# Kernel tuning notes

Measured on AMD Instinct MI355X. Metric: run time of the kernel, lower is better.

The kernel has to match this reference:

```python
import jax, jax.numpy as jnp
import numpy as np


def _log_g(x):
    # log of g(x) = x + 0.5 for x >= 0, sigmoid(x) for x < 0 (minGRU paper, log-space)
    return jnp.where(x >= 0, jnp.log(jax.nn.relu(x) + 0.5), -jax.nn.softplus(-x))


def setup_inputs() -> dict:
    key = jax.random.key(0)
    k1, k2, k3 = jax.random.split(key, 3)
    B, L, D, H = 4, 8192, 512, 1024
    x = jax.random.normal(k1, (B, L, D), dtype=jnp.float32)
    # 1x1 conv in-projection to [hidden | gate], scaled for sane activation magnitudes
    W_in = jax.random.normal(k2, (2 * H, D), dtype=jnp.float32) * 0.05
    b_in = jnp.zeros((2 * H,), dtype=jnp.float32)
    # 1x1 conv out-projection back to model dim
    W_out = jax.random.normal(k3, (D, H), dtype=jnp.float32) * 0.05
    b_out = jnp.zeros((D,), dtype=jnp.float32)
    return {"x": x, "W_in": W_in, "b_in": b_in, "W_out": W_out, "b_out": b_out}


def reference(x, W_in, b_in, W_out, b_out):
    # x: [B, L, D]. tokenMixer transposes to [B, D, L] for MinGRU (1x1 convs),
    # which is equivalent to pointwise matmuls over the channel dim here.
    hg = jnp.einsum('bld,ed->ble', x, W_in) + b_in          # [B, L, 2H]
    H = hg.shape[-1] // 2
    hidden, gate = hg[..., :H], hg[..., H:]

    # minGRU log-space parallel scan (Heinsen associative scan):
    # h_t = (1 - z_t) * h_{t-1} + z_t * g(hidden_t), z_t = sigmoid(gate_t)
    log_coeffs = -jax.nn.softplus(gate)      # log(1 - z_t)
    log_z = -jax.nn.softplus(-gate)          # log(z_t)
    log_tilde_h = _log_g(hidden)             # log(g(hidden_t))

    a_star = jnp.cumsum(log_coeffs, axis=1)                              # [B, L, H]
    log_h = a_star + jax.lax.cumlogsumexp(log_z + log_tilde_h - a_star, axis=1)
    h = jnp.exp(log_h)                                                   # [B, L, H]

    out = jnp.einsum('blh,dh->bld', h, W_out) + b_out                    # [B, L, D]
    return out
```

## Files before the change

### kernel.cpp

```cpp
#include <hip/hip_runtime.h>
#include <hip/hip_bf16.h>
#include <cstdint>
#include <cstddef>

#define B_ 4
#define L_ 8192
#define D_ 512
#define H_ 1024
#define NC_ 256
#define LC_ (L_ / NC_)

typedef float  f32x4 __attribute__((ext_vector_type(4)));
typedef short  s16x8 __attribute__((ext_vector_type(8)));
typedef __bf16 b16x8 __attribute__((ext_vector_type(8)));

template <typename T, typename U>
__device__ inline auto mfma_sel(T a, T b, f32x4 c, U, int)
    -> decltype(__builtin_amdgcn_mfma_f32_16x16x32_bf16(a, b, c, 0, 0, 0)) {
  return __builtin_amdgcn_mfma_f32_16x16x32_bf16(a, b, c, 0, 0, 0);
}
template <typename T, typename U>
__device__ inline f32x4 mfma_sel(T a, T b, f32x4 c, U, long) {
  return __builtin_amdgcn_mfma_f32_16x16x32_bf16(
      __builtin_bit_cast(U, a), __builtin_bit_cast(U, b), c, 0, 0, 0);
}
__device__ inline f32x4 mfma_bf16_16x16x32(s16x8 a, s16x8 b, f32x4 c) {
  return mfma_sel(a, b, c, b16x8{}, 0);
}

__device__ inline ushort f2bf(float f) {
  uint32_t u = __builtin_bit_cast(uint32_t, f);
  uint32_t r = (u + 0x7fffu + ((u >> 16) & 1u)) >> 16;
  return (ushort)r;
}
__device__ inline float bf2f(ushort u) {
  return __builtin_bit_cast(float, (uint32_t)u << 16);
}

__device__ inline float softplus_f(float x) {
  return fmaxf(x, 0.f) + __logf(1.f + __expf(-fabsf(x)));
}
__device__ inline float logaddexp_f(float a, float b) {
  float m = fmaxf(a, b);
  return m + __logf(1.f + __expf(-fabsf(a - b)));
}
__device__ inline void transform_f(float hd, float g, float& lc, float& v) {
  float sp = softplus_f(g);
  lc = -sp;
  float lz = g - sp;
  float lth = (hd >= 0.f) ? __logf(hd + 0.5f) : (hd - softplus_f(hd));
  v = lz + lth;
}

__global__ void cast_kernel(const float* __restrict__ in, ushort* __restrict__ out, int n4) {
  int i = blockIdx.x * blockDim.x + threadIdx.x;
  if (i >= n4) return;
  float4 f = reinterpret_cast<const float4*>(in)[i];
  ushort4 o;
  o.x = f2bf(f.x); o.y = f2bf(f.y); o.z = f2bf(f.z); o.w = f2bf(f.w);
  reinterpret_cast<ushort4*>(out)[i] = o;
}

__global__ void cast2_kernel(const float* __restrict__ in0, ushort* __restrict__ out0, int n4_0,
                             const float* __restrict__ in1, ushort* __restrict__ out1, int n4_1) {
  int i = blockIdx.x * blockDim.x + threadIdx.x;
  const float* in; ushort* out;
  if (i < n4_0) { in = in0; out = out0; }
  else { i -= n4_0; if (i >= n4_1) return; in = in1; out = out1; }
  float4 f = reinterpret_cast<const float4*>(in)[i];
  ushort4 o;
  o.x = f2bf(f.x); o.y = f2bf(f.y); o.z = f2bf(f.z); o.w = f2bf(f.w);
  reinterpret_cast<ushort4*>(out)[i] = o;
}

#define GLDS(srcp, dstp)                                                            \
  __builtin_amdgcn_global_load_lds(                                                 \
      (const __attribute__((address_space(1))) void*)(srcp),                        \
      (__attribute__((address_space(3))) void*)(dstp), 16, 0, 0)

template <int MODE, int KC>
__global__ __launch_bounds__(256, 3)
void gemm_bt(const ushort* __restrict__ A, const ushort* __restrict__ Bm,
             const float* __restrict__ bias, void* __restrict__ Cv,
             float* __restrict__ Acp, float* __restrict__ Bcp,
             int M, int N) {
  __shared__ ushort As[128 * 64];
  __shared__ ushort Bs[128 * 64];
  const int tid  = threadIdx.x;
  const int wave = tid >> 6;
  const int lane = tid & 63;
  const int l15  = lane & 15;
  const int quad = lane >> 4;

  int id = blockIdx.y * gridDim.x + blockIdx.x;
  const int nwg = gridDim.x * gridDim.y;
  id = (id & 7) * (nwg >> 3) + (id >> 3);
  const int bxi = id % gridDim.x;
  const int byi = id / gridDim.x;

  const long bm = (long)byi * 128;
  const int  wm = (wave >> 1) * 64;

  f32x4 acc[4][4];
#pragma unroll
  for (int i = 0; i < 4; ++i)
#pragma unroll
    for (int j = 0; j < 4; ++j) acc[i][j] = (f32x4){0.f, 0.f, 0.f, 0.f};

  const int rl  = lane >> 3;
  const int cb  = (lane & 7) ^ rl;
  const ushort* gA0 = A + (bm + wave * 32 + rl) * (long)KC + cb * 8;
  long bRowBase;
  if (MODE == 1) {
    const long n0 = (long)bxi * 64;
    bRowBase = (wave < 2) ? (n0 + wave * 32) : (1024 + n0 + (wave - 2) * 32);
  } else {
    bRowBase = (long)bxi * 128 + wave * 32;
  }
  const ushort* gB0 = Bm + (bRowBase + rl) * (long)KC + cb * 8;
  ushort* lA[4]; ushort* lB[4];
#pragma unroll
  for (int i = 0; i < 4; ++i) {
    lA[i] = &As[(wave * 32 + 8 * i) * 64];
    lB[i] = &Bs[(wave * 32 + 8 * i) * 64];
  }

  const int sq0 = ((0 * 4 + quad) ^ (l15 & 7)) * 8;
  const int sq1 = ((1 * 4 + quad) ^ (l15 & 7)) * 8;
  int arow[4], brow[4];
#pragma unroll
  for (int i = 0; i < 4; ++i) arow[i] = (wm + i * 16 + l15) * 64;
  if (MODE == 1) {
    const int wn0 = (wave & 1) * 32;
#pragma unroll
    for (int j = 0; j < 4; ++j) {
      const int trow = (j < 2) ? (wn0 + j * 16) : (64 + wn0 + (j - 2) * 16);
      brow[j] = (trow + l15) * 64;
    }
  } else {
    const int wn = (wave & 1) * 64;
#pragma unroll
    for (int j = 0; j < 4; ++j) brow[j] = (wn + j * 16 + l15) * 64;
  }

#pragma unroll
  for (int k0 = 0; k0 < KC; k0 += 64) {
#pragma unroll
    for (int i = 0; i < 4; ++i)
      GLDS(gA0 + 8L * i * KC + k0, lA[i]);
#pragma unroll
    for (int i = 0; i < 4; ++i)
      GLDS(gB0 + 8L * i * KC + k0, lB[i]);
    __syncthreads();

#pragma unroll
    for (int kh = 0; kh < 2; ++kh) {
      const int sq = kh ? sq1 : sq0;
      s16x8 af[4], bf[4];
#pragma unroll
      for (int mi = 0; mi < 4; ++mi)
        af[mi] = *reinterpret_cast<const s16x8*>(&As[arow[mi] + sq]);
#pragma unroll
      for (int ni = 0; ni < 4; ++ni)
        bf[ni] = *reinterpret_cast<const s16x8*>(&Bs[brow[ni] + sq]);
      __builtin_amdgcn_s_setprio(1);
#pragma unroll
      for (int mi = 0; mi < 4; ++mi)
#pragma unroll
        for (int ni = 0; ni < 4; ++ni)
          acc[mi][ni] = mfma_bf16_16x16x32(af[mi], bf[ni], acc[mi][ni]);
      __builtin_amdgcn_s_setprio(0);
    }
    __syncthreads();
  }

  if (MODE == 1) {
    const long n0  = (long)bxi * 64;
    const int  wn0 = (wave & 1) * 32;
    float ea[4][2], em[4][2], es[4][2];
#pragma unroll
    for (int mi = 0; mi < 4; ++mi) {
      const long mrow = bm + wm + mi * 16 + quad * 4;
#pragma unroll
      for (int j = 0; j < 2; ++j) {
        const long ch = n0 + wn0 + j * 16 + l15;
        const float bh = bias[ch];
        const float bg = bias[1024 + ch];
        ushort* lp = (ushort*)Cv + mrow * (long)N + ch;
        float lcr[4], vr[4];
#pragma unroll
        for (int r = 0; r < 4; ++r) {
          float hd = acc[mi][j][r] + bh;
          float g  = acc[mi][j + 2][r] + bg;
          transform_f(hd, g, lcr[r], vr[r]);
          lp[(long)r * N] = f2bf(lcr[r]);
          lp[(long)r * N + 1024] = f2bf(vr[r]);
        }
        float run = 0.f, ms = -INFINITY;
        float t0, t1, t2, t3;
        t3 = vr[3];            ms = t3;             run += lcr[3];
        t2 = vr[2] + run;      ms = fmaxf(ms, t2);  run += lcr[2];
        t1 = vr[1] + run;      ms = fmaxf(ms, t1);  run += lcr[1];
        t0 = vr[0] + run;      ms = fmaxf(ms, t0);  run += lcr[0];
        float ss = __expf(t0 - ms) + __expf(t1 - ms) + __expf(t2 - ms) + __expf(t3 - ms);
        ea[mi][j] = run; em[mi][j] = ms; es[mi][j] = ss;
      }
    }
#pragma unroll
    for (int j = 0; j < 2; ++j) {
#pragma unroll
      for (int cc = 0; cc < 2; ++cc) {
        const int mi0 = 2 * cc, mi1 = 2 * cc + 1;
        float suf0 = ea[mi0][j], suf1 = ea[mi1][j];
        { float tt = __shfl_down(suf0, 16); if (quad < 3) suf0 += tt;
          tt = __shfl_down(suf0, 32); if (quad < 2) suf0 += tt; }
        { float tt = __shfl_down(suf1, 16); if (quad < 3) suf1 += tt;
          tt = __shfl_down(suf1, 32); if (quad < 2) suf1 += tt; }
        const float tot0 = __shfl(suf0, l15);
        const float tot1 = __shfl(suf1, l15);
        float u0 = em[mi0][j] + (suf0 - ea[mi0][j]) + tot1;
        float u1 = em[mi1][j] + (suf1 - ea[mi1][j]);
        float Mx = fmaxf(u0, u1);
        Mx = fmaxf(Mx, __shfl_xor(Mx, 16));
        Mx = fmaxf(Mx, __shfl_xor(Mx, 32));
        float contrib = __expf(u0 - Mx) * es[mi0][j] + __expf(u1 - Mx) * es[mi1][j];
        contrib += __shfl_xor(contrib, 16);
        contrib += __shfl_xor(contrib, 32);
        if (quad == 0) {
          const long gc = (bm + wm + cc * 32) >> 5;
          const long ch = n0 + wn0 + j * 16 + l15;
          Acp[gc * H_ + ch] = tot0 + tot1;
          Bcp[gc * H_ + ch] = Mx + __logf(contrib);
        }
      }
    }
  } else {
    const int wn = (wave & 1) * 64;
#pragma unroll
    for (int mi = 0; mi < 4; ++mi) {
      const long mrow = bm + wm + mi * 16 + quad * 4;
#pragma unroll
      for (int ni = 0; ni < 4; ++ni) {
        const long ncol = (long)bxi * 128 + wn + ni * 16 + l15;
        const float bv = bias[ncol];
        float* cp = (float*)Cv + mrow * (long)N + ncol;
#pragma unroll
        for (int r = 0; r < 4; ++r) cp[(long)r * N] = acc[mi][ni][r] + bv;
      }
    }
  }
}

__global__ void scan_phase2(const float* __restrict__ Ac, const float* __restrict__ Bc,
                            float* __restrict__ carry) {
  const int wid  = (blockIdx.x * blockDim.x + threadIdx.x) >> 6;
  const int lane = threadIdx.x & 63;
  const int h = wid & (H_ - 1);
  const int b = wid >> 10;
  const size_t base = (size_t)b * NC_ * H_ + h;
  float pa[4], pb[4];
#pragma unroll
  for (int k = 0; k < 4; ++k) {
    size_t o = base + (size_t)(4 * lane + k) * H_;
    pa[k] = Ac[o]; pb[k] = Bc[o];
  }
  float sA = pa[0], sB = pb[0];
#pragma unroll
  for (int k = 1; k < 4; ++k) { sB = logaddexp_f(sB + pa[k], pb[k]); sA += pa[k]; }
  float iA = sA, iB = sB;
#pragma unroll
  for (int d = 1; d < 64; d <<= 1) {
    float uA = __shfl_up(iA, d);
    float uB = __shfl_up(iB, d);
    if (lane >= d) { iB = logaddexp_f(uB + iA, iB); iA = uA + iA; }
  }
  float eA = __shfl_up(iA, 1);
  float eB = __shfl_up(iB, 1);
  if (lane == 0) { eA = 0.f; eB = -INFINITY; }
  float Bst = eB;
#pragma unroll
  for (int k = 0; k < 4; ++k) {
    size_t o = base + (size_t)(4 * lane + k) * H_;
    carry[o] = Bst;
    Bst = logaddexp_f(Bst + pa[k], pb[k]);
  }
}

__global__ void scan_phase3(const ushort* __restrict__ hg, const float* __restrict__ carry,
                            ushort* __restrict__ hb) {
  int gid = blockIdx.x * blockDim.x + threadIdx.x;
  int hq = gid & (H_ / 4 - 1);
  int c  = (gid >> 8) & (NC_ - 1);
  int b  = gid >> 16;
  float4 cr = *reinterpret_cast<const float4*>(&carry[(size_t)(b * NC_ + c) * H_ + hq * 4]);
  float lh[4] = {cr.x, cr.y, cr.z, cr.w};
  const ushort* p = hg + ((size_t)(b * L_ + c * LC_) * (2 * H_)) + hq * 4;
  ushort* q = hb + (size_t)(b * L_ + c * LC_) * H_ + hq * 4;
#pragma unroll 4
  for (int l = 0; l < LC_; ++l) {
    ushort4 lc4 = *reinterpret_cast<const ushort4*>(p);
    ushort4 v4  = *reinterpret_cast<const ushort4*>(p + H_);
    float lcv[4] = {bf2f(lc4.x), bf2f(lc4.y), bf2f(lc4.z), bf2f(lc4.w)};
    float vv[4]  = {bf2f(v4.x),  bf2f(v4.y),  bf2f(v4.z),  bf2f(v4.w)};
    ushort4 o;
    ushort* op = &o.x;
#pragma unroll
    for (int j = 0; j < 4; ++j) {
      lh[j] = logaddexp_f(lh[j] + lcv[j], vv[j]);
      op[j] = f2bf(__expf(lh[j]));
    }
    *reinterpret_cast<ushort4*>(q) = o;
    p += 2 * H_;
    q += H_;
  }
}

extern "C" void kernel_launch(void* const* d_in, const int* in_sizes, int n_in,
                              void* d_out, int out_size, void* d_ws, size_t ws_size,
                              hipStream_t stream) {
  const float* x     = (const float*)d_in[0];
  const float* W_in  = (const float*)d_in[1];
  const float* b_in  = (const float*)d_in[2];
  const float* W_out = (const float*)d_in[3];
  const float* b_out = (const float*)d_in[4];
  float* out = (float*)d_out;

  char* ws = (char*)d_ws;
  size_t off = 0;
  auto alloc = [&](size_t bytes) {
    void* p = ws + off;
    off = (off + bytes + 255) & ~(size_t)255;
    return p;
  };
  ushort* xb    = (ushort*)alloc((size_t)B_ * L_ * H_ * 2);
  ushort* hb    = xb;
  ushort* Wib   = (ushort*)alloc((size_t)2 * H_ * D_ * 2);
  ushort* Wob   = (ushort*)alloc((size_t)D_ * H_ * 2);
  ushort* hgb   = (ushort*)alloc((size_t)B_ * L_ * 2 * H_ * 2);
  float*  Ac    = (float*)alloc((size_t)B_ * NC_ * H_ * 4);
  float*  Bc    = (float*)alloc((size_t)B_ * NC_ * H_ * 4);
  float*  carry = (float*)alloc((size_t)B_ * NC_ * H_ * 4);

  cast_kernel<<<(B_ * L_ * D_ / 4 + 255) / 256, 256, 0, stream>>>(x, xb, B_ * L_ * D_ / 4);
  {
    int n0 = 2 * H_ * D_ / 4, n1 = D_ * H_ / 4;
    cast2_kernel<<<(n0 + n1 + 255) / 256, 256, 0, stream>>>(W_in, Wib, n0, W_out, Wob, n1);
  }

  gemm_bt<1, 512><<<dim3(16, (B_ * L_) / 128), 256, 0, stream>>>(
      xb, Wib, b_in, hgb, Ac, Bc, B_ * L_, 2 * H_);

  scan_phase2<<<(B_ * H_ * 64) / 256, 256, 0, stream>>>(Ac, Bc, carry);
  scan_phase3<<<(B_ * NC_ * H_ / 4) / 256, 256, 0, stream>>>(hgb, carry, hb);

  gemm_bt<0, 1024><<<dim3(D_ / 128, (B_ * L_) / 128), 256, 0, stream>>>(
      hb, Wob, b_out, out, nullptr, nullptr, B_ * L_, D_);
}
```

Before: 346.0 us.

## Make GEMMs persistent with cross-tile prefetch and merge cast kernels

Both GEMM launches become persistent 768-block grids that loop over tile jobs. Each block issues the first k-slice of its next tile's global-to-LDS loads before running the current tile's epilogue, so load latency can overlap epilogue work and some launch and tail cost goes away. The three fp32-to-bf16 casts are merged into one launch. In exchange, the single LDS buffer is now refilled across the loop, which depends on careful sync ordering. With 768 blocks the second GEMM's 1024 jobs divide unevenly, so some blocks run two tiles and others one.

```diff
diff --git a/kernel.cpp b/kernel.cpp
--- a/kernel.cpp
+++ b/kernel.cpp
@@ -52,21 +52,17 @@
   v = lz + lth;
 }
 
-__global__ void cast_kernel(const float* __restrict__ in, ushort* __restrict__ out, int n4) {
-  int i = blockIdx.x * blockDim.x + threadIdx.x;
-  if (i >= n4) return;
-  float4 f = reinterpret_cast<const float4*>(in)[i];
-  ushort4 o;
-  o.x = f2bf(f.x); o.y = f2bf(f.y); o.z = f2bf(f.z); o.w = f2bf(f.w);
-  reinterpret_cast<ushort4*>(out)[i] = o;
-}
-
-__global__ void cast2_kernel(const float* __restrict__ in0, ushort* __restrict__ out0, int n4_0,
-                             const float* __restrict__ in1, ushort* __restrict__ out1, int n4_1) {
+__global__ void cast3_kernel(const float* __restrict__ in0, ushort* __restrict__ out0, int n0,
+                             const float* __restrict__ in1, ushort* __restrict__ out1, int n1,
+                             const float* __restrict__ in2, ushort* __restrict__ out2, int n2) {
   int i = blockIdx.x * blockDim.x + threadIdx.x;
   const float* in; ushort* out;
-  if (i < n4_0) { in = in0; out = out0; }
-  else { i -= n4_0; if (i >= n4_1) return; in = in1; out = out1; }
+  if (i < n0) { in = in0; out = out0; }
+  else {
+    i -= n0;
+    if (i < n1) { in = in1; out = out1; }
+    else { i -= n1; if (i >= n2) return; in = in2; out = out2; }
+  }
   float4 f = reinterpret_cast<const float4*>(in)[i];
   ushort4 o;
   o.x = f2bf(f.x); o.y = f2bf(f.y); o.z = f2bf(f.z); o.w = f2bf(f.w);
@@ -83,7 +79,7 @@
 void gemm_bt(const ushort* __restrict__ A, const ushort* __restrict__ Bm,
              const float* __restrict__ bias, void* __restrict__ Cv,
              float* __restrict__ Acp, float* __restrict__ Bcp,
-             int M, int N) {
+             int M, int N, int nbx, int njobs) {
   __shared__ ushort As[128 * 64];
   __shared__ ushort Bs[128 * 64];
   const int tid  = threadIdx.x;
@@ -91,33 +87,12 @@
   const int lane = tid & 63;
   const int l15  = lane & 15;
   const int quad = lane >> 4;
-
-  int id = blockIdx.y * gridDim.x + blockIdx.x;
-  const int nwg = gridDim.x * gridDim.y;
-  id = (id & 7) * (nwg >> 3) + (id >> 3);
-  const int bxi = id % gridDim.x;
-  const int byi = id / gridDim.x;
-
-  const long bm = (long)byi * 128;
-  const int  wm = (wave >> 1) * 64;
-
-  f32x4 acc[4][4];
-#pragma unroll
-  for (int i = 0; i < 4; ++i)
-#pragma unroll
-    for (int j = 0; j < 4; ++j) acc[i][j] = (f32x4){0.f, 0.f, 0.f, 0.f};
+  const int nblk = gridDim.x;
+
+  const int wm = (wave >> 1) * 64;
 
   const int rl  = lane >> 3;
   const int cb  = (lane & 7) ^ rl;
-  const ushort* gA0 = A + (bm + wave * 32 + rl) * (long)KC + cb * 8;
-  long bRowBase;
-  if (MODE == 1) {
-    const long n0 = (long)bxi * 64;
-    bRowBase = (wave < 2) ? (n0 + wave * 32) : (1024 + n0 + (wave - 2) * 32);
-  } else {
-    bRowBase = (long)bxi * 128 + wave * 32;
-  }
-  const ushort* gB0 = Bm + (bRowBase + rl) * (long)KC + cb * 8;
   ushort* lA[4]; ushort* lB[4];
 #pragma unroll
   for (int i = 0; i < 4; ++i) {
@@ -143,109 +118,156 @@
     for (int j = 0; j < 4; ++j) brow[j] = (wn + j * 16 + l15) * 64;
   }
 
-#pragma unroll
-  for (int k0 = 0; k0 < KC; k0 += 64) {
+  auto addrs = [&](int job, const ushort*& ga, const ushort*& gb) {
+    const int id  = (job & 7) * (njobs >> 3) + (job >> 3);
+    const int bxi = id % nbx;
+    const long bm = (long)(id / nbx) * 128;
+    ga = A + (bm + wave * 32 + rl) * (long)KC + cb * 8;
+    long bRowBase;
+    if (MODE == 1) {
+      const long n0 = (long)bxi * 64;
+      bRowBase = (wave < 2) ? (n0 + wave * 32) : (1024 + n0 + (wave - 2) * 32);
+    } else {
+      bRowBase = (long)bxi * 128 + wave * 32;
+    }
+    gb = Bm + (bRowBase + rl) * (long)KC + cb * 8;
+  };
+
+  const ushort *gA0, *gB0;
+  addrs(blockIdx.x, gA0, gB0);
+#pragma unroll
+  for (int i = 0; i < 4; ++i) GLDS(gA0 + 8L * i * KC, lA[i]);
+#pragma unroll
+  for (int i = 0; i < 4; ++i) GLDS(gB0 + 8L * i * KC, lB[i]);
+
+  for (int job = blockIdx.x; job < njobs; job += nblk) {
+    const int id  = (job & 7) * (njobs >> 3) + (job >> 3);
+    const int bxi = id % nbx;
+    const long bm = (long)(id / nbx) * 128;
+
+    f32x4 acc[4][4];
 #pragma unroll
     for (int i = 0; i < 4; ++i)
-      GLDS(gA0 + 8L * i * KC + k0, lA[i]);
-#pragma unroll
-    for (int i = 0; i < 4; ++i)
-      GLDS(gB0 + 8L * i * KC + k0, lB[i]);
-    __syncthreads();
-
-#pragma unroll
-    for (int kh = 0; kh < 2; ++kh) {
-      const int sq = kh ? sq1 : sq0;
-      s16x8 af[4], bf[4];
-#pragma unroll
-      for (int mi = 0; mi < 4; ++mi)
-        af[mi] = *reinterpret_cast<const s16x8*>(&As[arow[mi] + sq]);
-#pragma unroll
-      for (int ni = 0; ni < 4; ++ni)
-        bf[ni] = *reinterpret_cast<const s16x8*>(&Bs[brow[ni] + sq]);
-      __builtin_amdgcn_s_setprio(1);
-#pragma unroll
-      for (int mi = 0; mi < 4; ++mi)
+#pragma unroll
+      for (int j = 0; j < 4; ++j) acc[i][j] = (f32x4){0.f, 0.f, 0.f, 0.f};
+
+    const ushort *gAn = gA0, *gBn = gB0;
+
+#pragma unroll
+    for (int k0 = 0; k0 < KC; k0 += 64) {
+      __syncthreads();
+
+#pragma unroll
+      for (int kh = 0; kh < 2; ++kh) {
+        const int sq = kh ? sq1 : sq0;
+        s16x8 af[4], bf[4];
+#pragma unroll
+        for (int mi = 0; mi < 4; ++mi)
+          af[mi] = *reinterpret_cast<const s16x8*>(&As[arow[mi] + sq]);
 #pragma unroll
         for (int ni = 0; ni < 4; ++ni)
-          acc[mi][ni] = mfma_bf16_16x16x32(af[mi], bf[ni], acc[mi][ni]);
-      __builtin_amdgcn_s_setprio(0);
-    }
-    __syncthreads();
-  }
-
-  if (MODE == 1) {
-    const long n0  = (long)bxi * 64;
-    const int  wn0 = (wave & 1) * 32;
-    float ea[4][2], em[4][2], es[4][2];
-#pragma unroll
-    for (int mi = 0; mi < 4; ++mi) {
-      const long mrow = bm + wm + mi * 16 + quad * 4;
+          bf[ni] = *reinterpret_cast<const s16x8*>(&Bs[brow[ni] + sq]);
+        __builtin_amdgcn_s_setprio(1);
+#pragma unroll
+        for (int mi = 0; mi < 4; ++mi)
+#pragma unroll
+          for (int ni = 0; ni < 4; ++ni)
+            acc[mi][ni] = mfma_bf16_16x16x32(af[mi], bf[ni], acc[mi][ni]);
+        __builtin_amdgcn_s_setprio(0);
+      }
+      __syncthreads();
+
+      if (k0 + 64 < KC) {
+#pragma unroll
+        for (int i = 0; i < 4; ++i) GLDS(gA0 + 8L * i * KC + (k0 + 64), lA[i]);
+#pragma unroll
+        for (int i = 0; i < 4; ++i) GLDS(gB0 + 8L * i * KC + (k0 + 64), lB[i]);
+      } else {
+        const int nj = job + nblk;
+        if (nj < njobs) {
+          addrs(nj, gAn, gBn);
+#pragma unroll
+          for (int i = 0; i < 4; ++i) GLDS(gAn + 8L * i * KC, lA[i]);
+#pragma unroll
+          for (int i = 0; i < 4; ++i) GLDS(gBn + 8L * i * KC, lB[i]);
+        }
+      }
+    }
+    gA0 = gAn; gB0 = gBn;
+
+    if (MODE == 1) {
+      const long n0  = (long)bxi * 64;
+      const int  wn0 = (wave & 1) * 32;
+      float ea[4][2], em[4][2], es[4][2];
+#pragma unroll
+      for (int mi = 0; mi < 4; ++mi) {
+        const long mrow = bm + wm + mi * 16 + quad * 4;
+#pragma unroll
+        for (int j = 0; j < 2; ++j) {
+          const long ch = n0 + wn0 + j * 16 + l15;
+          const float bh = bias[ch];
+          const float bg = bias[1024 + ch];
+          ushort* lp = (ushort*)Cv + mrow * (long)N + ch;
+          float lcr[4], vr[4];
+#pragma unroll
+          for (int r = 0; r < 4; ++r) {
+            float hd = acc[mi][j][r] + bh;
+            float g  = acc[mi][j + 2][r] + bg;
+            transform_f(hd, g, lcr[r], vr[r]);
+            lp[(long)r * N] = f2bf(lcr[r]);
+            lp[(long)r * N + 1024] = f2bf(vr[r]);
+          }
+          float run = 0.f, ms = -INFINITY;
+          float t0, t1, t2, t3;
+          t3 = vr[3];            ms = t3;             run += lcr[3];
+          t2 = vr[2] + run;      ms = fmaxf(ms, t2);  run += lcr[2];
+          t1 = vr[1] + run;      ms = fmaxf(ms, t1);  run += lcr[1];
+          t0 = vr[0] + run;      ms = fmaxf(ms, t0);  run += lcr[0];
+          float ss = __expf(t0 - ms) + __expf(t1 - ms) + __expf(t2 - ms) + __expf(t3 - ms);
+          ea[mi][j] = run; em[mi][j] = ms; es[mi][j] = ss;
+        }
+      }
 #pragma unroll
       for (int j = 0; j < 2; ++j) {
-        const long ch = n0 + wn0 + j * 16 + l15;
-        const float bh = bias[ch];
-        const float bg = bias[1024 + ch];
-        ushort* lp = (ushort*)Cv + mrow * (long)N + ch;
-        float lcr[4], vr[4];
-#pragma unroll
-        for (int r = 0; r < 4; ++r) {
-          float hd = acc[mi][j][r] + bh;
-          float g  = acc[mi][j + 2][r] + bg;
-          transform_f(hd, g, lcr[r], vr[r]);
-          lp[(long)r * N] = f2bf(lcr[r]);
-          lp[(long)r * N + 1024] = f2bf(vr[r]);
+#pragma unroll
+        for (int cc = 0; cc < 2; ++cc) {
+          const int mi0 = 2 * cc, mi1 = 2 * cc + 1;
+          float suf0 = ea[mi0][j], suf1 = ea[mi1][j];
+          { float tt = __shfl_down(suf0, 16); if (quad < 3) suf0 += tt;
+            tt = __shfl_down(suf0, 32); if (quad < 2) suf0 += tt; }
+          { float tt = __shfl_down(suf1, 16); if (quad < 3) suf1 += tt;
+            tt = __shfl_down(suf1, 32); if (quad < 2) suf1 += tt; }
+          const float tot0 = __shfl(suf0, l15);
+          const float tot1 = __shfl(suf1, l15);
+          float u0 = em[mi0][j] + (suf0 - ea[mi0][j]) + tot1;
+          float u1 = em[mi1][j] + (suf1 - ea[mi1][j]);
+          float Mx = fmaxf(u0, u1);
+          Mx = fmaxf(Mx, __shfl_xor(Mx, 16));
+          Mx = fmaxf(Mx, __shfl_xor(Mx, 32));
+          float contrib = __expf(u0 - Mx) * es[mi0][j] + __expf(u1 - Mx) * es[mi1][j];
+          contrib += __shfl_xor(contrib, 16);
+          contrib += __shfl_xor(contrib, 32);
+          if (quad == 0) {
+            const long gc = (bm + wm + cc * 32) >> 5;
+            const long ch = n0 + wn0 + j * 16 + l15;
+            Acp[gc * H_ + ch] = tot0 + tot1;
+            Bcp[gc * H_ + ch] = Mx + __logf(contrib);
+          }
         }
-        float run = 0.f, ms = -INFINITY;
-        float t0, t1, t2, t3;
-        t3 = vr[3];            ms = t3;             run += lcr[3];
-        t2 = vr[2] + run;      ms = fmaxf(ms, t2);  run += lcr[2];
-        t1 = vr[1] + run;      ms = fmaxf(ms, t1);  run += lcr[1];
-        t0 = vr[0] + run;      ms = fmaxf(ms, t0);  run += lcr[0];
-        float ss = __expf(t0 - ms) + __expf(t1 - ms) + __expf(t2 - ms) + __expf(t3 - ms);
-        ea[mi][j] = run; em[mi][j] = ms; es[mi][j] = ss;
-      }
-    }
-#pragma unroll
-    for (int j = 0; j < 2; ++j) {
-#pragma unroll
-      for (int cc = 0; cc < 2; ++cc) {
-        const int mi0 = 2 * cc, mi1 = 2 * cc + 1;
-        float suf0 = ea[mi0][j], suf1 = ea[mi1][j];
-        { float tt = __shfl_down(suf0, 16); if (quad < 3) suf0 += tt;
-          tt = __shfl_down(suf0, 32); if (quad < 2) suf0 += tt; }
-        { float tt = __shfl_down(suf1, 16); if (quad < 3) suf1 += tt;
-          tt = __shfl_down(suf1, 32); if (quad < 2) suf1 += tt; }
-        const float tot0 = __shfl(suf0, l15);
-        const float tot1 = __shfl(suf1, l15);
-        float u0 = em[mi0][j] + (suf0 - ea[mi0][j]) + tot1;
-        float u1 = em[mi1][j] + (suf1 - ea[mi1][j]);
-        float Mx = fmaxf(u0, u1);
-        Mx = fmaxf(Mx, __shfl_xor(Mx, 16));
-        Mx = fmaxf(Mx, __shfl_xor(Mx, 32));
-        float contrib = __expf(u0 - Mx) * es[mi0][j] + __expf(u1 - Mx) * es[mi1][j];
-        contrib += __shfl_xor(contrib, 16);
-        contrib += __shfl_xor(contrib, 32);
-        if (quad == 0) {
-          const long gc = (bm + wm + cc * 32) >> 5;
-          const long ch = n0 + wn0 + j * 16 + l15;
-          Acp[gc * H_ + ch] = tot0 + tot1;
-          Bcp[gc * H_ + ch] = Mx + __logf(contrib);
+      }
+    } else {
+      const int wn = (wave & 1) * 64;
+#pragma unroll
+      for (int mi = 0; mi < 4; ++mi) {
+        const long mrow = bm + wm + mi * 16 + quad * 4;
+#pragma unroll
+        for (int ni = 0; ni < 4; ++ni) {
+          const long ncol = (long)bxi * 128 + wn + ni * 16 + l15;
+          const float bv = bias[ncol];
+          float* cp = (float*)Cv + mrow * (long)N + ncol;
+#pragma unroll
+          for (int r = 0; r < 4; ++r) cp[(long)r * N] = acc[mi][ni][r] + bv;
         }
-      }
-    }
-  } else {
-    const int wn = (wave & 1) * 64;
-#pragma unroll
-    for (int mi = 0; mi < 4; ++mi) {
-      const long mrow = bm + wm + mi * 16 + quad * 4;
-#pragma unroll
-      for (int ni = 0; ni < 4; ++ni) {
-        const long ncol = (long)bxi * 128 + wn + ni * 16 + l15;
-        const float bv = bias[ncol];
-        float* cp = (float*)Cv + mrow * (long)N + ncol;
-#pragma unroll
-        for (int r = 0; r < 4; ++r) cp[(long)r * N] = acc[mi][ni][r] + bv;
       }
     }
   }
@@ -341,18 +363,18 @@
   float*  Bc    = (float*)alloc((size_t)B_ * NC_ * H_ * 4);
   float*  carry = (float*)alloc((size_t)B_ * NC_ * H_ * 4);
 
-  cast_kernel<<<(B_ * L_ * D_ / 4 + 255) / 256, 256, 0, stream>>>(x, xb, B_ * L_ * D_ / 4);
   {
-    int n0 = 2 * H_ * D_ / 4, n1 = D_ * H_ / 4;
-    cast2_kernel<<<(n0 + n1 + 255) / 256, 256, 0, stream>>>(W_in, Wib, n0, W_out, Wob, n1);
-  }
-
-  gemm_bt<1, 512><<<dim3(16, (B_ * L_) / 128), 256, 0, stream>>>(
-      xb, Wib, b_in, hgb, Ac, Bc, B_ * L_, 2 * H_);
+    int n0 = B_ * L_ * D_ / 4, n1 = 2 * H_ * D_ / 4, n2 = D_ * H_ / 4;
+    cast3_kernel<<<(n0 + n1 + n2 + 255) / 256, 256, 0, stream>>>(
+        x, xb, n0, W_in, Wib, n1, W_out, Wob, n2);
+  }
+
+  gemm_bt<1, 512><<<768, 256, 0, stream>>>(
+      xb, Wib, b_in, hgb, Ac, Bc, B_ * L_, 2 * H_, 16, 4096);
 
   scan_phase2<<<(B_ * H_ * 64) / 256, 256, 0, stream>>>(Ac, Bc, carry);
   scan_phase3<<<(B_ * NC_ * H_ / 4) / 256, 256, 0, stream>>>(hgb, carry, hb);
 
-  gemm_bt<0, 1024><<<dim3(D_ / 128, (B_ * L_) / 128), 256, 0, stream>>>(
-      hb, Wob, b_out, out, nullptr, nullptr, B_ * L_, D_);
-}
+  gemm_bt<0, 1024><<<768, 256, 0, stream>>>(
+      hb, Wob, b_out, out, nullptr, nullptr, B_ * L_, D_, 4, 1024);
+}
```

Result: no change. 345.2 us (-0.2%).
